# Optimization experiments

Measured on AMD Instinct MI355X. Metric: run time of the kernel, lower is better.

The kernel has to match this reference:

```python
import jax, jax.numpy as jnp
import numpy as np

GATE_SCALE = 1.7015  # logistic-probit approximation constant


def setup_inputs() -> dict:
    key = jax.random.key(0)
    k1, k2, k3, k4, k5 = jax.random.split(key, 5)
    B, S, D = 2, 1024, 1024
    Bs = 8
    N = D // Bs
    x_real = jax.random.normal(k1, (B, S, D), dtype=jnp.float32)
    x_imag = jax.random.normal(k2, (B, S, D), dtype=jnp.float32)
    A_real = jax.random.normal(k3, (N, Bs, Bs), dtype=jnp.float32) * 0.02
    A_imag = jax.random.normal(k4, (N, Bs, Bs), dtype=jnp.float32) * 0.02
    W_gate = jax.random.normal(k5, (D, 2 * D), dtype=jnp.float32) * (1.0 / np.sqrt(2 * D))
    b_gate = jnp.zeros((D,), dtype=jnp.float32)
    return {"x_real": x_real, "x_imag": x_imag, "A_real": A_real, "A_imag": A_imag,
            "W_gate": W_gate, "b_gate": b_gate}


def reference(x_real, x_imag, A_real, A_imag, W_gate, b_gate):
    B, S, D = x_real.shape
    N, Bs, _ = A_real.shape
    # per-feature gate from concatenated real/imag parts
    x_cat = jnp.concatenate([x_real, x_imag], axis=-1)  # [B,S,2D]
    gate = jax.nn.sigmoid((x_cat @ W_gate.T + b_gate) * GATE_SCALE)  # [B,S,D]
    g_block = gate.reshape(B, S, N, Bs).mean(axis=-1)[..., None, None]  # [B,S,N,1,1]
    # enforce anti-Hermitian generator: A_r skew-symmetric, A_i symmetric
    A_r = (A_real - jnp.swapaxes(A_real, -2, -1)) * 0.5
    A_i = (A_imag + jnp.swapaxes(A_imag, -2, -1)) * 0.5
    gA_r = g_block * A_r  # [B,S,N,Bs,Bs]
    gA_i = g_block * A_i
    eye = jnp.eye(Bs, dtype=x_real.dtype)
    IpA_r = eye + gA_r
    ImA_r = eye - gA_r
    # real-block isomorphism: 2Bs x 2Bs real system per block
    LHS = jnp.concatenate([
        jnp.concatenate([IpA_r, -gA_i], axis=-1),
        jnp.concatenate([gA_i, IpA_r], axis=-1)], axis=-2)  # [B,S,N,2Bs,2Bs]
    RHS = jnp.concatenate([
        jnp.concatenate([ImA_r, gA_i], axis=-1),
        jnp.concatenate([-gA_i, ImA_r], axis=-1)], axis=-2)
    U_rb = jnp.linalg.solve(LHS, RHS)  # batched over [B,S,N]
    U_real = U_rb[..., :Bs, :Bs]
    U_imag = U_rb[..., Bs:, :Bs]
    xr = x_real.reshape(B, S, N, Bs)
    xi = x_imag.reshape(B, S, N, Bs)
    out_real = jnp.einsum('bsnoi,bsni->bsno', U_real, xr) - jnp.einsum('bsnoi,bsni->bsno', U_imag, xi)
    out_imag = jnp.einsum('bsnoi,bsni->bsno', U_real, xi) + jnp.einsum('bsnoi,bsni->bsno', U_imag, xr)
    # complex output represented as stacked (real, imag): [2,B,S,D]
    return jnp.stack([out_real.reshape(B, S, D), out_imag.reshape(B, S, D)], axis=0)
```

## Files before the change

kernel.cpp:

```cpp
#include <hip/hip_runtime.h>

#define GATE_SCALE 1.7015f
#define SX 32.0f
#define SW 1024.0f
#define DESCALE 3.0517578125e-05f

typedef __attribute__((ext_vector_type(4))) int   v4i;
typedef __attribute__((ext_vector_type(16))) int  v16i;

__device__ __forceinline__ void gl2lds16(const void* g, void* l) {
    __builtin_amdgcn_global_load_lds((const __attribute__((address_space(1))) void*)g,
                                     (__attribute__((address_space(3))) void*)l, 16, 0, 0);
}

__device__ __forceinline__ int q8(float v, float s) {
    int q = __float2int_rn(v * s);
    return q < -127 ? -127 : (q > 127 ? 127 : q);
}

__global__ void convert_kernel(const float* __restrict__ xr, const float* __restrict__ xi,
                               const float* __restrict__ W,
                               const float* __restrict__ Ar, const float* __restrict__ Ai,
                               signed char* __restrict__ xq, signed char* __restrict__ wq,
                               float* __restrict__ Ac) {
    int bx = blockIdx.x;
    if (bx >= 1024) {
        int v = (bx - 1024) * 256 + threadIdx.x;
        if (v < 8192) {
            int n = v >> 6, t = v & 63, o = t >> 3, i = t & 7;
            const float* arn = Ar + n * 64;
            const float* ain = Ai + n * 64;
            float a_r = 0.5f * (arn[o * 8 + i] - arn[i * 8 + o]);
            float a_i = 0.5f * (ain[o * 8 + i] + ain[i * 8 + o]);
            Ac[n * 128 + t * 2]     = a_r;
            Ac[n * 128 + t * 2 + 1] = a_i;
        }
        return;
    }
    const int XCV = 2048 * 2048 / 4;
    const int WV  = 1024 * 2048 / 4;
    const int STR = 1024 * 256;
    for (int v = bx * 256 + threadIdx.x; v < XCV + WV; v += STR) {
        float4 f;
        signed char* dst;
        float s;
        if (v < XCV) {
            int idx = v * 4;
            int m = idx >> 11;
            int k = idx & 2047;
            const float* src = (k < 1024) ? (xr + m * 1024 + k) : (xi + m * 1024 + k - 1024);
            f = *(const float4*)src;
            dst = xq + idx;
            s = SX;
        } else {
            int idx = (v - XCV) * 4;
            f = *(const float4*)(W + idx);
            dst = wq + idx;
            s = SW;
        }
        int a = q8(f.x, s), b = q8(f.y, s), c = q8(f.z, s), d = q8(f.w, s);
        unsigned int packed = (a & 0xFF) | ((b & 0xFF) << 8) | ((c & 0xFF) << 16)
                            | ((unsigned)(d & 0xFF) << 24);
        *(unsigned int*)dst = packed;
    }
}

__launch_bounds__(256, 2)
__global__ void gemm_gate_kernel(const signed char* __restrict__ A,
                                 const signed char* __restrict__ Bw,
                                 const float* __restrict__ bias,
                                 float* __restrict__ g) {
    __shared__ __align__(16) signed char lA[4][64 * 128];
    __shared__ __align__(16) signed char lB[4][64 * 128];
    const int tid = threadIdx.x;
    const int lane = tid & 63;
    const int wid = tid >> 6;
    const int bid = blockIdx.x;
    const int x = bid & 7, l = bid >> 3;
    const int m0 = ((x & 3) * 8 + (l & 7)) * 64;
    const int n0 = ((x >> 2) * 8 + (l >> 3)) * 64;
    const int wr = wid >> 1, wc = wid & 1;
    const int lo = lane & 31, hi = lane >> 5, lo3 = lane & 7;
    const int arow = wr * 32 + lo, brow = wc * 32 + lo;
    const int ar7 = arow & 7, br7 = brow & 7;

    v16i acc = {};

    #define STAGE(buf, k0)                                                          \
        {                                                                           \
            _Pragma("unroll")                                                       \
            for (int q = 0; q < 2; ++q) {                                           \
                int c = q * 256 + tid;                                              \
                int row = c >> 3, ks = (c & 7) ^ (row & 7);                         \
                gl2lds16(&A[(m0 + row) * 2048 + (k0) + ks * 16], &lA[buf][c * 16]); \
            }                                                                       \
            _Pragma("unroll")                                                       \
            for (int q = 0; q < 2; ++q) {                                           \
                int c = q * 256 + tid;                                              \
                int row = c >> 3, ks = (c & 7) ^ (row & 7);                         \
                gl2lds16(&Bw[(n0 + row) * 2048 + (k0) + ks * 16], &lB[buf][c * 16]);\
            }                                                                       \
        }

    #define TILE(t, vmstr, do_stage)                                               \
        {                                                                           \
            asm volatile("s_waitcnt vmcnt(" vmstr ")" ::: "memory");                \
            __builtin_amdgcn_s_barrier();                                           \
            const int b = (t) & 3;                                                  \
            v4i af[4], bf[4];                                                       \
            _Pragma("unroll")                                                       \
            for (int kk = 0; kk < 4; ++kk) {                                        \
                const int ch = ((2 * kk + hi) ^ ar7) << 4;                          \
                const int chb = ((2 * kk + hi) ^ br7) << 4;                         \
                af[kk] = *(const v4i*)&lA[b][arow * 128 + ch];                      \
                bf[kk] = *(const v4i*)&lB[b][brow * 128 + chb];                     \
            }                                                                       \
            if (do_stage) STAGE((((t) + 3) & 3), ((t) + 3) * 128);                  \
            __builtin_amdgcn_s_setprio(1);                                          \
            _Pragma("unroll")                                                       \
            for (int kk = 0; kk < 4; ++kk)                                          \
                acc = __builtin_amdgcn_mfma_i32_32x32x32_i8(af[kk], bf[kk], acc, 0, 0, 0); \
            __builtin_amdgcn_s_setprio(0);                                          \
        }

    STAGE(0, 0);
    STAGE(1, 128);
    STAGE(2, 256);
    for (int t = 0; t < 13; ++t) TILE(t, "8", true);
    TILE(13, "8", false);
    TILE(14, "4", false);
    TILE(15, "0", false);
    #undef TILE
    #undef STAGE

    const int ncol = n0 + wc * 32 + lo;
    const float bv = bias[ncol];
    const int gcol = ncol >> 3;
    #pragma unroll
    for (int r = 0; r < 16; ++r) {
        const int mrow = m0 + wr * 32 + (r & 3) + 8 * (r >> 2) + 4 * hi;
        float z = ((float)acc[r] * DESCALE + bv) * GATE_SCALE;
        float gate = 1.0f / (1.0f + __expf(-z));
        gate += __shfl_xor(gate, 1);
        gate += __shfl_xor(gate, 2);
        gate += __shfl_xor(gate, 4);
        if (lo3 == 0)
            g[mrow * 128 + gcol] = gate * 0.125f;
    }
}

__launch_bounds__(256)
__global__ void apply_kernel(const float* __restrict__ xr, const float* __restrict__ xi,
                             const float* __restrict__ g,
                             const float* __restrict__ Ac,
                             float* __restrict__ outr, float* __restrict__ outi) {
    const int tid = threadIdx.x;
    const int lane = tid & 63;
    const int wv = tid >> 6;
    const int nl = lane >> 1, h = lane & 1;
    const int n = blockIdx.x * 32 + nl;
    const int mbase = blockIdx.y * 8 + wv * 2;

    float Ar_[4][8], Ai_[4][8];
    const float* An = Ac + n * 128;
    #pragma unroll
    for (int r = 0; r < 4; ++r) {
        const int o = h * 4 + r;
        #pragma unroll
        for (int p = 0; p < 2; ++p) {
            float4 f = *(const float4*)&An[o * 16 + h * 8 + p * 4];
            Ar_[r][p * 2]     = f.x;  Ai_[r][p * 2]     = f.y;
            Ar_[r][p * 2 + 1] = f.z;  Ai_[r][p * 2 + 1] = f.w;
        }
        #pragma unroll
        for (int p = 0; p < 2; ++p) {
            float4 f = *(const float4*)&An[o * 16 + (1 - h) * 8 + p * 4];
            Ar_[r][4 + p * 2]     = f.x;  Ai_[r][4 + p * 2]     = f.y;
            Ar_[r][4 + p * 2 + 1] = f.z;  Ai_[r][4 + p * 2 + 1] = f.w;
        }
    }

    #define CMV()                                                                   \
        {                                                                           \
            float pwr[4], pwi[4];                                                   \
            _Pragma("unroll")                                                       \
            for (int k2 = 0; k2 < 4; ++k2) {                                        \
                pwr[k2] = __shfl_xor(wr[k2], 1);                                    \
                pwi[k2] = __shfl_xor(wi[k2], 1);                                    \
            }                                                                       \
            _Pragma("unroll")                                                       \
            for (int r = 0; r < 4; ++r) {                                           \
                float sr = 0.f, si = 0.f;                                           \
                _Pragma("unroll")                                                   \
                for (int jj = 0; jj < 4; ++jj) {                                    \
                    sr += Ar_[r][jj] * wr[jj]      - Ai_[r][jj] * wi[jj];           \
                    si += Ar_[r][jj] * wi[jj]      + Ai_[r][jj] * wr[jj];           \
                    sr += Ar_[r][4 + jj] * pwr[jj] - Ai_[r][4 + jj] * pwi[jj];      \
                    si += Ar_[r][4 + jj] * pwi[jj] + Ai_[r][4 + jj] * pwr[jj];      \
                }                                                                   \
                tr[r] = sr; ti[r] = si;                                             \
            }                                                                       \
        }

    #pragma unroll
    for (int mi = 0; mi < 2; ++mi) {
        const int m = mbase + mi;
        const int d = n * 8 + h * 4;
        const float4 fvr = *(const float4*)&xr[m * 1024 + d];
        const float4 fvi = *(const float4*)&xi[m * 1024 + d];
        float vr[4] = {fvr.x, fvr.y, fvr.z, fvr.w};
        float vi[4] = {fvi.x, fvi.y, fvi.z, fvi.w};
        const float gv = g[m * 128 + n];
        const float c1 = -2.f * gv, c2 = -c1 * gv, c3 = -c2 * gv, c4 = -c3 * gv;
        float wr[4], wi[4], tr[4], ti[4];

        #pragma unroll
        for (int r = 0; r < 4; ++r) { wr[r] = c4 * vr[r]; wi[r] = c4 * vi[r]; }
        CMV();
        #pragma unroll
        for (int r = 0; r < 4; ++r) { wr[r] = c3 * vr[r] + tr[r]; wi[r] = c3 * vi[r] + ti[r]; }
        CMV();
        #pragma unroll
        for (int r = 0; r < 4; ++r) { wr[r] = c2 * vr[r] + tr[r]; wi[r] = c2 * vi[r] + ti[r]; }
        CMV();
        #pragma unroll
        for (int r = 0; r < 4; ++r) { wr[r] = c1 * vr[r] + tr[r]; wi[r] = c1 * vi[r] + ti[r]; }
        CMV();

        float4 s0 = {vr[0] + tr[0], vr[1] + tr[1], vr[2] + tr[2], vr[3] + tr[3]};
        float4 s1 = {vi[0] + ti[0], vi[1] + ti[1], vi[2] + ti[2], vi[3] + ti[3]};
        *(float4*)&outr[m * 1024 + d] = s0;
        *(float4*)&outi[m * 1024 + d] = s1;
    }
    #undef CMV
}

extern "C" void kernel_launch(void* const* d_in, const int* in_sizes, int n_in,
                              void* d_out, int out_size, void* d_ws, size_t ws_size,
                              hipStream_t stream) {
    const float* xr = (const float*)d_in[0];
    const float* xi = (const float*)d_in[1];
    const float* Ar = (const float*)d_in[2];
    const float* Ai = (const float*)d_in[3];
    const float* W  = (const float*)d_in[4];
    const float* bg = (const float*)d_in[5];
    float* out = (float*)d_out;

    char* ws = (char*)d_ws;
    signed char* xq = (signed char*)(ws);
    signed char* wq = (signed char*)(ws + 4194304);
    float*  g  = (float*)(ws + 6291456);
    float*  Ac = (float*)(ws + 7340032);

    hipLaunchKernelGGL(convert_kernel, dim3(1056), dim3(256), 0, stream,
                       xr, xi, W, Ar, Ai, xq, wq, Ac);
    hipLaunchKernelGGL(gemm_gate_kernel, dim3(512), dim3(256), 0, stream, xq, wq, bg, g);
    hipLaunchKernelGGL(apply_kernel, dim3(4, 256), dim3(256), 0, stream,
                       xr, xi, g, Ac, out, out + 2 * 1024 * 1024);
}
```

Measured before the change: 38.99 us.

## Split K across two wave groups in gate GEMM with LDS reduction

Doubles the GEMM block to 512 threads. Two groups of four waves each take half of every 128-wide K tile, and the partial accumulators are reduced through LDS before the sigmoid epilogue. Staging loads are spread over twice as many threads, so each thread issues one load per matrix and the vmcnt waits are halved. The aim is more waves in flight to hide load and MFMA latency. The cost is an extra LDS reduction with two barriers, and possibly lower occupancy with 64KB of LDS per block.

```diff
diff --git a/kernel.cpp b/kernel.cpp
--- a/kernel.cpp
+++ b/kernel.cpp
@@ -65,7 +65,7 @@
     }
 }
 
-__launch_bounds__(256, 2)
+__launch_bounds__(512, 4)
 __global__ void gemm_gate_kernel(const signed char* __restrict__ A,
                                  const signed char* __restrict__ Bw,
                                  const float* __restrict__ bias,
@@ -79,27 +79,19 @@
     const int x = bid & 7, l = bid >> 3;
     const int m0 = ((x & 3) * 8 + (l & 7)) * 64;
     const int n0 = ((x >> 2) * 8 + (l >> 3)) * 64;
-    const int wr = wid >> 1, wc = wid & 1;
+    const int wm = (wid >> 1) & 1, wn = wid & 1, kg = wid >> 2;
     const int lo = lane & 31, hi = lane >> 5, lo3 = lane & 7;
-    const int arow = wr * 32 + lo, brow = wc * 32 + lo;
+    const int arow = wm * 32 + lo, brow = wn * 32 + lo;
     const int ar7 = arow & 7, br7 = brow & 7;
 
     v16i acc = {};
 
     #define STAGE(buf, k0)                                                          \
         {                                                                           \
-            _Pragma("unroll")                                                       \
-            for (int q = 0; q < 2; ++q) {                                           \
-                int c = q * 256 + tid;                                              \
-                int row = c >> 3, ks = (c & 7) ^ (row & 7);                         \
-                gl2lds16(&A[(m0 + row) * 2048 + (k0) + ks * 16], &lA[buf][c * 16]); \
-            }                                                                       \
-            _Pragma("unroll")                                                       \
-            for (int q = 0; q < 2; ++q) {                                           \
-                int c = q * 256 + tid;                                              \
-                int row = c >> 3, ks = (c & 7) ^ (row & 7);                         \
-                gl2lds16(&Bw[(n0 + row) * 2048 + (k0) + ks * 16], &lB[buf][c * 16]);\
-            }                                                                       \
+            { int c = tid; int row = c >> 3, ks = (c & 7) ^ (row & 7);              \
+              gl2lds16(&A[(m0 + row) * 2048 + (k0) + ks * 16], &lA[buf][c * 16]); } \
+            { int c = tid; int row = c >> 3, ks = (c & 7) ^ (row & 7);              \
+              gl2lds16(&Bw[(n0 + row) * 2048 + (k0) + ks * 16], &lB[buf][c * 16]); }\
         }
 
     #define TILE(t, vmstr, do_stage)                                               \
@@ -107,18 +99,17 @@
             asm volatile("s_waitcnt vmcnt(" vmstr ")" ::: "memory");                \
             __builtin_amdgcn_s_barrier();                                           \
             const int b = (t) & 3;                                                  \
-            v4i af[4], bf[4];                                                       \
-            _Pragma("unroll")                                                       \
-            for (int kk = 0; kk < 4; ++kk) {                                        \
-                const int ch = ((2 * kk + hi) ^ ar7) << 4;                          \
-                const int chb = ((2 * kk + hi) ^ br7) << 4;                         \
-                af[kk] = *(const v4i*)&lA[b][arow * 128 + ch];                      \
-                bf[kk] = *(const v4i*)&lB[b][brow * 128 + chb];                     \
+            v4i af[2], bf[2];                                                       \
+            _Pragma("unroll")                                                       \
+            for (int kk = 0; kk < 2; ++kk) {                                        \
+                const int kx = 2 * (kk + 2 * kg) + hi;                              \
+                af[kk] = *(const v4i*)&lA[b][arow * 128 + ((kx ^ ar7) << 4)];       \
+                bf[kk] = *(const v4i*)&lB[b][brow * 128 + ((kx ^ br7) << 4)];       \
             }                                                                       \
             if (do_stage) STAGE((((t) + 3) & 3), ((t) + 3) * 128);                  \
             __builtin_amdgcn_s_setprio(1);                                          \
             _Pragma("unroll")                                                       \
-            for (int kk = 0; kk < 4; ++kk)                                          \
+            for (int kk = 0; kk < 2; ++kk)                                          \
                 acc = __builtin_amdgcn_mfma_i32_32x32x32_i8(af[kk], bf[kk], acc, 0, 0, 0); \
             __builtin_amdgcn_s_setprio(0);                                          \
         }
@@ -126,26 +117,40 @@
     STAGE(0, 0);
     STAGE(1, 128);
     STAGE(2, 256);
-    for (int t = 0; t < 13; ++t) TILE(t, "8", true);
-    TILE(13, "8", false);
-    TILE(14, "4", false);
+    for (int t = 0; t < 13; ++t) TILE(t, "4", true);
+    TILE(13, "4", false);
+    TILE(14, "2", false);
     TILE(15, "0", false);
     #undef TILE
     #undef STAGE
 
-    const int ncol = n0 + wc * 32 + lo;
-    const float bv = bias[ncol];
-    const int gcol = ncol >> 3;
-    #pragma unroll
-    for (int r = 0; r < 16; ++r) {
-        const int mrow = m0 + wr * 32 + (r & 3) + 8 * (r >> 2) + 4 * hi;
-        float z = ((float)acc[r] * DESCALE + bv) * GATE_SCALE;
-        float gate = 1.0f / (1.0f + __expf(-z));
-        gate += __shfl_xor(gate, 1);
-        gate += __shfl_xor(gate, 2);
-        gate += __shfl_xor(gate, 4);
-        if (lo3 == 0)
-            g[mrow * 128 + gcol] = gate * 0.125f;
+    __syncthreads();
+    int* red = (int*)&lA[0][0];
+    if (kg == 1) {
+        #pragma unroll
+        for (int r = 0; r < 16; ++r)
+            red[(wid & 3) * 1024 + r * 64 + lane] = acc[r];
+    }
+    __syncthreads();
+    if (kg == 0) {
+        #pragma unroll
+        for (int r = 0; r < 16; ++r)
+            acc[r] += red[(wid & 3) * 1024 + r * 64 + lane];
+
+        const int ncol = n0 + wn * 32 + lo;
+        const float bv = bias[ncol];
+        const int gcol = ncol >> 3;
+        #pragma unroll
+        for (int r = 0; r < 16; ++r) {
+            const int mrow = m0 + wm * 32 + (r & 3) + 8 * (r >> 2) + 4 * hi;
+            float z = ((float)acc[r] * DESCALE + bv) * GATE_SCALE;
+            float gate = 1.0f / (1.0f + __expf(-z));
+            gate += __shfl_xor(gate, 1);
+            gate += __shfl_xor(gate, 2);
+            gate += __shfl_xor(gate, 4);
+            if (lo3 == 0)
+                g[mrow * 128 + gcol] = gate * 0.125f;
+        }
     }
 }
 
@@ -254,7 +259,7 @@
 
     hipLaunchKernelGGL(convert_kernel, dim3(1056), dim3(256), 0, stream,
                        xr, xi, W, Ar, Ai, xq, wq, Ac);
-    hipLaunchKernelGGL(gemm_gate_kernel, dim3(512), dim3(256), 0, stream, xq, wq, bg, g);
+    hipLaunchKernelGGL(gemm_gate_kernel, dim3(512), dim3(512), 0, stream, xq, wq, bg, g);
     hipLaunchKernelGGL(apply_kernel, dim3(4, 256), dim3(256), 0, stream,
                        xr, xi, g, Ac, out, out + 2 * 1024 * 1024);
 }
```

Result: slower. 39.82 us (+2.1%).

## Pre-tile int8 operands into MFMA fragment layout and load directly to registers

Applied to the files above, without the earlier changes.

The convert kernel now writes the quantized x and W in a blocked layout where each 32-row group stores the 16-byte fragments each lane needs for the 32x32x32 int8 MFMA contiguously. The GEMM kernel drops the LDS staging, the barriers and the swizzle, and loads fragments straight from global memory into registers with double buffering. This removes LDS traffic and synchronisation, but gives up LDS-based reuse across waves: each wave re-reads its A and B panels from L2/global, and the launch bound no longer asks for two blocks per SIMD.

```diff
diff --git a/kernel.cpp b/kernel.cpp
--- a/kernel.cpp
+++ b/kernel.cpp
@@ -8,11 +8,6 @@
 typedef __attribute__((ext_vector_type(4))) int   v4i;
 typedef __attribute__((ext_vector_type(16))) int  v16i;
 
-__device__ __forceinline__ void gl2lds16(const void* g, void* l) {
-    __builtin_amdgcn_global_load_lds((const __attribute__((address_space(1))) void*)g,
-                                     (__attribute__((address_space(3))) void*)l, 16, 0, 0);
-}
-
 __device__ __forceinline__ int q8(float v, float s) {
     int q = __float2int_rn(v * s);
     return q < -127 ? -127 : (q > 127 ? 127 : q);
@@ -21,7 +16,7 @@
 __global__ void convert_kernel(const float* __restrict__ xr, const float* __restrict__ xi,
                                const float* __restrict__ W,
                                const float* __restrict__ Ar, const float* __restrict__ Ai,
-                               signed char* __restrict__ xq, signed char* __restrict__ wq,
+                               signed char* __restrict__ xqt, signed char* __restrict__ wqt,
                                float* __restrict__ Ac) {
     int bx = blockIdx.x;
     if (bx >= 1024) {
@@ -42,36 +37,42 @@
     const int STR = 1024 * 256;
     for (int v = bx * 256 + threadIdx.x; v < XCV + WV; v += STR) {
         float4 f;
-        signed char* dst;
+        signed char* base;
+        int row, k;
         float s;
         if (v < XCV) {
             int idx = v * 4;
-            int m = idx >> 11;
-            int k = idx & 2047;
-            const float* src = (k < 1024) ? (xr + m * 1024 + k) : (xi + m * 1024 + k - 1024);
+            row = idx >> 11;
+            k = idx & 2047;
+            const float* src = (k < 1024) ? (xr + row * 1024 + k)
+                                          : (xi + row * 1024 + k - 1024);
             f = *(const float4*)src;
-            dst = xq + idx;
+            base = xqt;
             s = SX;
         } else {
             int idx = (v - XCV) * 4;
-            f = *(const float4*)(W + idx);
-            dst = wq + idx;
+            row = idx >> 11;
+            k = idx & 2047;
+            f = *(const float4*)(W + row * 2048 + k);
+            base = wqt;
             s = SW;
         }
         int a = q8(f.x, s), b = q8(f.y, s), c = q8(f.z, s), d = q8(f.w, s);
         unsigned int packed = (a & 0xFF) | ((b & 0xFF) << 8) | ((c & 0xFF) << 16)
                             | ((unsigned)(d & 0xFF) << 24);
-        *(unsigned int*)dst = packed;
-    }
-}
-
-__launch_bounds__(256, 2)
-__global__ void gemm_gate_kernel(const signed char* __restrict__ A,
-                                 const signed char* __restrict__ Bw,
+        const int g = row >> 5, lo = row & 31;
+        const int kx = k >> 4;
+        const int off = g * 65536 + (kx >> 1) * 1024 + (kx & 1) * 512
+                      + lo * 16 + (k & 15);
+        *(unsigned int*)(base + off) = packed;
+    }
+}
+
+__launch_bounds__(256)
+__global__ void gemm_gate_kernel(const signed char* __restrict__ At,
+                                 const signed char* __restrict__ Bt,
                                  const float* __restrict__ bias,
                                  float* __restrict__ g) {
-    __shared__ __align__(16) signed char lA[4][64 * 128];
-    __shared__ __align__(16) signed char lB[4][64 * 128];
     const int tid = threadIdx.x;
     const int lane = tid & 63;
     const int wid = tid >> 6;
@@ -81,57 +82,38 @@
     const int n0 = ((x >> 2) * 8 + (l >> 3)) * 64;
     const int wr = wid >> 1, wc = wid & 1;
     const int lo = lane & 31, hi = lane >> 5, lo3 = lane & 7;
-    const int arow = wr * 32 + lo, brow = wc * 32 + lo;
-    const int ar7 = arow & 7, br7 = brow & 7;
+
+    const signed char* pa = At + ((m0 >> 5) + wr) * 65536 + lane * 16;
+    const signed char* pb = Bt + ((n0 >> 5) + wc) * 65536 + lane * 16;
 
     v16i acc = {};
-
-    #define STAGE(buf, k0)                                                          \
-        {                                                                           \
-            _Pragma("unroll")                                                       \
-            for (int q = 0; q < 2; ++q) {                                           \
-                int c = q * 256 + tid;                                              \
-                int row = c >> 3, ks = (c & 7) ^ (row & 7);                         \
-                gl2lds16(&A[(m0 + row) * 2048 + (k0) + ks * 16], &lA[buf][c * 16]); \
-            }                                                                       \
-            _Pragma("unroll")                                                       \
-            for (int q = 0; q < 2; ++q) {                                           \
-                int c = q * 256 + tid;                                              \
-                int row = c >> 3, ks = (c & 7) ^ (row & 7);                         \
-                gl2lds16(&Bw[(n0 + row) * 2048 + (k0) + ks * 16], &lB[buf][c * 16]);\
-            }                                                                       \
-        }
-
-    #define TILE(t, vmstr, do_stage)                                               \
-        {                                                                           \
-            asm volatile("s_waitcnt vmcnt(" vmstr ")" ::: "memory");                \
-            __builtin_amdgcn_s_barrier();                                           \
-            const int b = (t) & 3;                                                  \
-            v4i af[4], bf[4];                                                       \
-            _Pragma("unroll")                                                       \
-            for (int kk = 0; kk < 4; ++kk) {                                        \
-                const int ch = ((2 * kk + hi) ^ ar7) << 4;                          \
-                const int chb = ((2 * kk + hi) ^ br7) << 4;                         \
-                af[kk] = *(const v4i*)&lA[b][arow * 128 + ch];                      \
-                bf[kk] = *(const v4i*)&lB[b][brow * 128 + chb];                     \
-            }                                                                       \
-            if (do_stage) STAGE((((t) + 3) & 3), ((t) + 3) * 128);                  \
-            __builtin_amdgcn_s_setprio(1);                                          \
-            _Pragma("unroll")                                                       \
-            for (int kk = 0; kk < 4; ++kk)                                          \
-                acc = __builtin_amdgcn_mfma_i32_32x32x32_i8(af[kk], bf[kk], acc, 0, 0, 0); \
-            __builtin_amdgcn_s_setprio(0);                                          \
-        }
-
-    STAGE(0, 0);
-    STAGE(1, 128);
-    STAGE(2, 256);
-    for (int t = 0; t < 13; ++t) TILE(t, "8", true);
-    TILE(13, "8", false);
-    TILE(14, "4", false);
-    TILE(15, "0", false);
-    #undef TILE
-    #undef STAGE
+    v4i a0[4], b0[4], a1[4], b1[4];
+    #pragma unroll
+    for (int j = 0; j < 4; ++j) {
+        a0[j] = *(const v4i*)(pa + j * 1024);
+        b0[j] = *(const v4i*)(pb + j * 1024);
+    }
+    #pragma unroll
+    for (int kp = 0; kp < 16; kp += 2) {
+        #pragma unroll
+        for (int j = 0; j < 4; ++j) {
+            a1[j] = *(const v4i*)(pa + ((kp + 1) * 4 + j) * 1024);
+            b1[j] = *(const v4i*)(pb + ((kp + 1) * 4 + j) * 1024);
+        }
+        #pragma unroll
+        for (int j = 0; j < 4; ++j)
+            acc = __builtin_amdgcn_mfma_i32_32x32x32_i8(a0[j], b0[j], acc, 0, 0, 0);
+        if (kp < 14) {
+            #pragma unroll
+            for (int j = 0; j < 4; ++j) {
+                a0[j] = *(const v4i*)(pa + ((kp + 2) * 4 + j) * 1024);
+                b0[j] = *(const v4i*)(pb + ((kp + 2) * 4 + j) * 1024);
+            }
+        }
+        #pragma unroll
+        for (int j = 0; j < 4; ++j)
+            acc = __builtin_amdgcn_mfma_i32_32x32x32_i8(a1[j], b1[j], acc, 0, 0, 0);
+    }
 
     const int ncol = n0 + wc * 32 + lo;
     const float bv = bias[ncol];
@@ -247,14 +229,14 @@
     float* out = (float*)d_out;
 
     char* ws = (char*)d_ws;
-    signed char* xq = (signed char*)(ws);
-    signed char* wq = (signed char*)(ws + 4194304);
+    signed char* xqt = (signed char*)(ws);
+    signed char* wqt = (signed char*)(ws + 4194304);
     float*  g  = (float*)(ws + 6291456);
     float*  Ac = (float*)(ws + 7340032);
 
     hipLaunchKernelGGL(convert_kernel, dim3(1056), dim3(256), 0, stream,
-                       xr, xi, W, Ar, Ai, xq, wq, Ac);
-    hipLaunchKernelGGL(gemm_gate_kernel, dim3(512), dim3(256), 0, stream, xq, wq, bg, g);
+                       xr, xi, W, Ar, Ai, xqt, wqt, Ac);
+    hipLaunchKernelGGL(gemm_gate_kernel, dim3(512), dim3(256), 0, stream, xqt, wqt, bg, g);
     hipLaunchKernelGGL(apply_kernel, dim3(4, 256), dim3(256), 0, stream,
                        xr, xi, g, Ac, out, out + 2 * 1024 * 1024);
 }
```

New measurement: 45.40 us. 16.4% more time.

## Fuse gate GEMM epilogue with Cayley apply stage via LDS gate tile

Applied to the files above, without the earlier changes.

The gate GEMM and the block-wise Cayley apply kernel are merged into one kernel. Each GEMM tile writes its 64x8 block-mean gate values to shared memory, synchronizes, then applies the 8x8 complex transform to the matching 64 rows by 64 features of x. This removes one kernel launch and the global round trip of the gate array. In exchange the apply work runs inside the GEMM's occupancy and register limits, which could raise register pressure or lengthen the tail of the GEMM kernel.

```diff
diff --git a/kernel.cpp b/kernel.cpp
--- a/kernel.cpp
+++ b/kernel.cpp
@@ -48,7 +48,8 @@
             int idx = v * 4;
             int m = idx >> 11;
             int k = idx & 2047;
-            const float* src = (k < 1024) ? (xr + m * 1024 + k) : (xi + m * 1024 + k - 1024);
+            const float* src = (k < 1024) ? (xr + m * 1024 + k)
+                                          : (xi + m * 1024 + k - 1024);
             f = *(const float4*)src;
             dst = xq + idx;
             s = SX;
@@ -66,10 +67,12 @@
 }
 
 __launch_bounds__(256, 2)
-__global__ void gemm_gate_kernel(const signed char* __restrict__ A,
-                                 const signed char* __restrict__ Bw,
-                                 const float* __restrict__ bias,
-                                 float* __restrict__ g) {
+__global__ void gemm_apply_kernel(const signed char* __restrict__ A,
+                                  const signed char* __restrict__ Bw,
+                                  const float* __restrict__ bias,
+                                  const float* __restrict__ xr, const float* __restrict__ xi,
+                                  const float* __restrict__ Ac,
+                                  float* __restrict__ outr, float* __restrict__ outi) {
     __shared__ __align__(16) signed char lA[4][64 * 128];
     __shared__ __align__(16) signed char lB[4][64 * 128];
     const int tid = threadIdx.x;
@@ -133,106 +136,103 @@
     #undef TILE
     #undef STAGE
 
-    const int ncol = n0 + wc * 32 + lo;
-    const float bv = bias[ncol];
-    const int gcol = ncol >> 3;
-    #pragma unroll
-    for (int r = 0; r < 16; ++r) {
-        const int mrow = m0 + wr * 32 + (r & 3) + 8 * (r >> 2) + 4 * hi;
-        float z = ((float)acc[r] * DESCALE + bv) * GATE_SCALE;
-        float gate = 1.0f / (1.0f + __expf(-z));
-        gate += __shfl_xor(gate, 1);
-        gate += __shfl_xor(gate, 2);
-        gate += __shfl_xor(gate, 4);
-        if (lo3 == 0)
-            g[mrow * 128 + gcol] = gate * 0.125f;
-    }
-}
-
-__launch_bounds__(256)
-__global__ void apply_kernel(const float* __restrict__ xr, const float* __restrict__ xi,
-                             const float* __restrict__ g,
-                             const float* __restrict__ Ac,
-                             float* __restrict__ outr, float* __restrict__ outi) {
-    const int tid = threadIdx.x;
-    const int lane = tid & 63;
-    const int wv = tid >> 6;
-    const int nl = lane >> 1, h = lane & 1;
-    const int n = blockIdx.x * 32 + nl;
-    const int mbase = blockIdx.y * 8 + wv * 2;
-
-    float Ar_[4][8], Ai_[4][8];
-    const float* An = Ac + n * 128;
-    #pragma unroll
-    for (int r = 0; r < 4; ++r) {
-        const int o = h * 4 + r;
+    float* lds_g = (float*)&lA[0][0];
+    {
+        const int ncol = n0 + wc * 32 + lo;
+        const float bv = bias[ncol];
+        const int gl = wc * 4 + (lo >> 3);
         #pragma unroll
-        for (int p = 0; p < 2; ++p) {
-            float4 f = *(const float4*)&An[o * 16 + h * 8 + p * 4];
-            Ar_[r][p * 2]     = f.x;  Ai_[r][p * 2]     = f.y;
-            Ar_[r][p * 2 + 1] = f.z;  Ai_[r][p * 2 + 1] = f.w;
-        }
+        for (int r = 0; r < 16; ++r) {
+            const int mloc = wr * 32 + (r & 3) + 8 * (r >> 2) + 4 * hi;
+            float z = ((float)acc[r] * DESCALE + bv) * GATE_SCALE;
+            float gate = 1.0f / (1.0f + __expf(-z));
+            gate += __shfl_xor(gate, 1);
+            gate += __shfl_xor(gate, 2);
+            gate += __shfl_xor(gate, 4);
+            if (lo3 == 0)
+                lds_g[mloc * 8 + gl] = gate * 0.125f;
+        }
+    }
+    __syncthreads();
+
+    {
+        const int h = tid & 1, j = (tid >> 1) & 7, mb = tid >> 4;
+        const int n = (n0 >> 3) + j;
+
+        float Ar_[4][8], Ai_[4][8];
+        const float* An = Ac + n * 128;
         #pragma unroll
-        for (int p = 0; p < 2; ++p) {
-            float4 f = *(const float4*)&An[o * 16 + (1 - h) * 8 + p * 4];
-            Ar_[r][4 + p * 2]     = f.x;  Ai_[r][4 + p * 2]     = f.y;
-            Ar_[r][4 + p * 2 + 1] = f.z;  Ai_[r][4 + p * 2 + 1] = f.w;
-        }
-    }
-
-    #define CMV()                                                                   \
-        {                                                                           \
-            float pwr[4], pwi[4];                                                   \
-            _Pragma("unroll")                                                       \
-            for (int k2 = 0; k2 < 4; ++k2) {                                        \
-                pwr[k2] = __shfl_xor(wr[k2], 1);                                    \
-                pwi[k2] = __shfl_xor(wi[k2], 1);                                    \
-            }                                                                       \
-            _Pragma("unroll")                                                       \
-            for (int r = 0; r < 4; ++r) {                                           \
-                float sr = 0.f, si = 0.f;                                           \
-                _Pragma("unroll")                                                   \
-                for (int jj = 0; jj < 4; ++jj) {                                    \
-                    sr += Ar_[r][jj] * wr[jj]      - Ai_[r][jj] * wi[jj];           \
-                    si += Ar_[r][jj] * wi[jj]      + Ai_[r][jj] * wr[jj];           \
-                    sr += Ar_[r][4 + jj] * pwr[jj] - Ai_[r][4 + jj] * pwi[jj];      \
-                    si += Ar_[r][4 + jj] * pwi[jj] + Ai_[r][4 + jj] * pwr[jj];      \
-                }                                                                   \
-                tr[r] = sr; ti[r] = si;                                             \
-            }                                                                       \
-        }
-
-    #pragma unroll
-    for (int mi = 0; mi < 2; ++mi) {
-        const int m = mbase + mi;
-        const int d = n * 8 + h * 4;
-        const float4 fvr = *(const float4*)&xr[m * 1024 + d];
-        const float4 fvi = *(const float4*)&xi[m * 1024 + d];
-        float vr[4] = {fvr.x, fvr.y, fvr.z, fvr.w};
-        float vi[4] = {fvi.x, fvi.y, fvi.z, fvi.w};
-        const float gv = g[m * 128 + n];
-        const float c1 = -2.f * gv, c2 = -c1 * gv, c3 = -c2 * gv, c4 = -c3 * gv;
-        float wr[4], wi[4], tr[4], ti[4];
+        for (int r = 0; r < 4; ++r) {
+            const int o = h * 4 + r;
+            #pragma unroll
+            for (int p = 0; p < 2; ++p) {
+                float4 f = *(const float4*)&An[o * 16 + h * 8 + p * 4];
+                Ar_[r][p * 2]     = f.x;  Ai_[r][p * 2]     = f.y;
+                Ar_[r][p * 2 + 1] = f.z;  Ai_[r][p * 2 + 1] = f.w;
+            }
+            #pragma unroll
+            for (int p = 0; p < 2; ++p) {
+                float4 f = *(const float4*)&An[o * 16 + (1 - h) * 8 + p * 4];
+                Ar_[r][4 + p * 2]     = f.x;  Ai_[r][4 + p * 2]     = f.y;
+                Ar_[r][4 + p * 2 + 1] = f.z;  Ai_[r][4 + p * 2 + 1] = f.w;
+            }
+        }
+
+        #define CMV()                                                                   \
+            {                                                                           \
+                float pwr[4], pwi[4];                                                   \
+                _Pragma("unroll")                                                       \
+                for (int k2 = 0; k2 < 4; ++k2) {                                        \
+                    pwr[k2] = __shfl_xor(wr[k2], 1);                                    \
+                    pwi[k2] = __shfl_xor(wi[k2], 1);                                    \
+                }                                                                       \
+                _Pragma("unroll")                                                       \
+                for (int r = 0; r < 4; ++r) {                                           \
+                    float sr = 0.f, si = 0.f;                                           \
+                    _Pragma("unroll")                                                   \
+                    for (int jj = 0; jj < 4; ++jj) {                                    \
+                        sr += Ar_[r][jj] * wr[jj]      - Ai_[r][jj] * wi[jj];           \
+                        si += Ar_[r][jj] * wi[jj]      + Ai_[r][jj] * wr[jj];           \
+                        sr += Ar_[r][4 + jj] * pwr[jj] - Ai_[r][4 + jj] * pwi[jj];      \
+                        si += Ar_[r][4 + jj] * pwi[jj] + Ai_[r][4 + jj] * pwr[jj];      \
+                    }                                                                   \
+                    tr[r] = sr; ti[r] = si;                                             \
+                }                                                                       \
+            }
 
         #pragma unroll
-        for (int r = 0; r < 4; ++r) { wr[r] = c4 * vr[r]; wi[r] = c4 * vi[r]; }
-        CMV();
-        #pragma unroll
-        for (int r = 0; r < 4; ++r) { wr[r] = c3 * vr[r] + tr[r]; wi[r] = c3 * vi[r] + ti[r]; }
-        CMV();
-        #pragma unroll
-        for (int r = 0; r < 4; ++r) { wr[r] = c2 * vr[r] + tr[r]; wi[r] = c2 * vi[r] + ti[r]; }
-        CMV();
-        #pragma unroll
-        for (int r = 0; r < 4; ++r) { wr[r] = c1 * vr[r] + tr[r]; wi[r] = c1 * vi[r] + ti[r]; }
-        CMV();
-
-        float4 s0 = {vr[0] + tr[0], vr[1] + tr[1], vr[2] + tr[2], vr[3] + tr[3]};
-        float4 s1 = {vi[0] + ti[0], vi[1] + ti[1], vi[2] + ti[2], vi[3] + ti[3]};
-        *(float4*)&outr[m * 1024 + d] = s0;
-        *(float4*)&outi[m * 1024 + d] = s1;
-    }
-    #undef CMV
+        for (int mi = 0; mi < 4; ++mi) {
+            const int mloc = mb + mi * 16;
+            const int m = m0 + mloc;
+            const int d = n * 8 + h * 4;
+            const float4 fvr = *(const float4*)&xr[m * 1024 + d];
+            const float4 fvi = *(const float4*)&xi[m * 1024 + d];
+            float vr[4] = {fvr.x, fvr.y, fvr.z, fvr.w};
+            float vi[4] = {fvi.x, fvi.y, fvi.z, fvi.w};
+            const float gv = lds_g[mloc * 8 + j];
+            const float c1 = -2.f * gv, c2 = -c1 * gv, c3 = -c2 * gv, c4 = -c3 * gv;
+            float wr[4], wi[4], tr[4], ti[4];
+
+            #pragma unroll
+            for (int r = 0; r < 4; ++r) { wr[r] = c4 * vr[r]; wi[r] = c4 * vi[r]; }
+            CMV();
+            #pragma unroll
+            for (int r = 0; r < 4; ++r) { wr[r] = c3 * vr[r] + tr[r]; wi[r] = c3 * vi[r] + ti[r]; }
+            CMV();
+            #pragma unroll
+            for (int r = 0; r < 4; ++r) { wr[r] = c2 * vr[r] + tr[r]; wi[r] = c2 * vi[r] + ti[r]; }
+            CMV();
+            #pragma unroll
+            for (int r = 0; r < 4; ++r) { wr[r] = c1 * vr[r] + tr[r]; wi[r] = c1 * vi[r] + ti[r]; }
+            CMV();
+
+            float4 s0 = {vr[0] + tr[0], vr[1] + tr[1], vr[2] + tr[2], vr[3] + tr[3]};
+            float4 s1 = {vi[0] + ti[0], vi[1] + ti[1], vi[2] + ti[2], vi[3] + ti[3]};
+            *(float4*)&outr[m * 1024 + d] = s0;
+            *(float4*)&outi[m * 1024 + d] = s1;
+        }
+        #undef CMV
+    }
 }
 
 extern "C" void kernel_launch(void* const* d_in, const int* in_sizes, int n_in,
@@ -249,12 +249,10 @@
     char* ws = (char*)d_ws;
     signed char* xq = (signed char*)(ws);
     signed char* wq = (signed char*)(ws + 4194304);
-    float*  g  = (float*)(ws + 6291456);
-    float*  Ac = (float*)(ws + 7340032);
+    float*  Ac = (float*)(ws + 6291456);
 
     hipLaunchKernelGGL(convert_kernel, dim3(1056), dim3(256), 0, stream,
                        xr, xi, W, Ar, Ai, xq, wq, Ac);
-    hipLaunchKernelGGL(gemm_gate_kernel, dim3(512), dim3(256), 0, stream, xq, wq, bg, g);
-    hipLaunchKernelGGL(apply_kernel, dim3(4, 256), dim3(256), 0, stream,
-                       xr, xi, g, Ac, out, out + 2 * 1024 * 1024);
-}
+    hipLaunchKernelGGL(gemm_apply_kernel, dim3(512), dim3(256), 0, stream,
+                       xq, wq, bg, xr, xi, Ac, out, out + 2 * 1024 * 1024);
+}
```

After: 35.01 us. -10.2%, faster.
